# Optimization experiments

Hardware: AMD Instinct MI355X
Metric: run time of the kernel (lower is better)

The kernel has to match this reference:

```python
import jax, jax.numpy as jnp
import numpy as np

NEG_SLOPE = 0.2  # PyG GATConv default

def gat_layer(x, src, dst, W, a_src, a_dst, b, N):
    # h = W x  (PyG applies linear before attention)
    h = x @ W                                   # [N, hid]
    al_src = h @ a_src                          # [N]
    al_dst = h @ a_dst                          # [N]
    e = jax.nn.leaky_relu(al_src[src] + al_dst[dst], NEG_SLOPE)  # [E]
    # segment softmax over incoming edges of each destination node
    m = jax.ops.segment_max(e, dst, num_segments=N)
    e = jnp.exp(e - m[dst])
    s = jax.ops.segment_sum(e, dst, num_segments=N)
    coef = e / s[dst]                           # [E]
    out = jax.ops.segment_sum(h[src] * coef[:, None], dst, num_segments=N)
    return out + b

def setup_inputs() -> dict:
    key = jax.random.key(0)
    ks = jax.random.split(key, 12)
    N, E, in_dim, hid, out_dim, G = 100000, 1600000, 128, 64, 1, 256
    x = jax.random.normal(ks[0], (N, in_dim), dtype=jnp.float32)
    edge_index = jax.random.randint(ks[1], (2, E), 0, N, dtype=jnp.int64)
    batch = jnp.sort(jax.random.randint(ks[2], (N,), 0, G, dtype=jnp.int64))
    def glorot(k, shape):
        lim = float(np.sqrt(6.0 / (shape[0] + shape[-1])))
        return jax.random.uniform(k, shape, jnp.float32, -lim, lim)
    return {
        "x": x, "edge_index": edge_index, "batch": batch,
        "W1": glorot(ks[3], (in_dim, hid)),
        "a_src1": glorot(ks[4], (hid,)), "a_dst1": glorot(ks[5], (hid,)),
        "b1": jnp.zeros((hid,), jnp.float32),
        "W2": glorot(ks[6], (hid, hid)),
        "a_src2": glorot(ks[7], (hid,)), "a_dst2": glorot(ks[8], (hid,)),
        "b2": jnp.zeros((hid,), jnp.float32),
        "Wfc": glorot(ks[9], (hid, out_dim)),
        "bfc": jnp.zeros((out_dim,), jnp.float32),
    }

def reference(x, edge_index, batch, W1, a_src1, a_dst1, b1, W2, a_src2, a_dst2, b2, Wfc, bfc):
    N = x.shape[0]
    G = 256  # number of graphs in the batch
    # add self-loops (PyG GATConv default add_self_loops=True)
    loops = jnp.arange(N, dtype=edge_index.dtype)
    src = jnp.concatenate([edge_index[0], loops])
    dst = jnp.concatenate([edge_index[1], loops])
    h = jax.nn.elu(gat_layer(x, src, dst, W1, a_src1, a_dst1, b1, N))
    h = jax.nn.elu(gat_layer(h, src, dst, W2, a_src2, a_dst2, b2, N))
    # global mean pool over graph ids
    sums = jax.ops.segment_sum(h, batch, num_segments=G)
    cnts = jax.ops.segment_sum(jnp.ones((N,), h.dtype), batch, num_segments=G)
    pooled = sums / jnp.maximum(cnts, 1.0)[:, None]
    return pooled @ Wfc + bfc
```

## Files before the change

### kernel.cpp

```cpp
#include <hip/hip_runtime.h>
#include <hip/hip_bf16.h>
#include <cstdint>


#define BIN_SHIFT 8
#define BIN_NODES 256
#define PLACE_CHUNK 8192

__device__ __forceinline__ float wave_reduce_sum(float v) {
#pragma unroll
  for (int off = 32; off > 0; off >>= 1) v += __shfl_xor(v, off, 64);
  return v;
}

__device__ __forceinline__ unsigned short f2bf(float f) {
  unsigned int u = __float_as_uint(f);
  u += 0x7fffu + ((u >> 16) & 1u);
  return (unsigned short)(u >> 16);
}
__device__ __forceinline__ float bf2f(unsigned short u) {
  return __uint_as_float(((unsigned int)u) << 16);
}


__global__ void bin_count_kernel(const int* __restrict__ ei, int E, int M, int NB,
                                 int* __restrict__ binCnt) {
  extern __shared__ int hist[];
  for (int i = threadIdx.x; i < NB; i += blockDim.x) hist[i] = 0;
  __syncthreads();
  int stride = gridDim.x * blockDim.x;
  for (int t = blockIdx.x * blockDim.x + threadIdx.x; t < M; t += stride) {
    int d = (t < E) ? ei[E + t] : (t - E);
    atomicAdd(&hist[d >> BIN_SHIFT], 1);
  }
  __syncthreads();
  for (int i = threadIdx.x; i < NB; i += blockDim.x)
    if (hist[i]) atomicAdd(&binCnt[i], hist[i]);
}

__global__ void scan_bounds_kernel(const int* __restrict__ binCnt, int NB,
                                   int* __restrict__ binBase, int* __restrict__ binCursor,
                                   const int* __restrict__ batch, int* __restrict__ gstart,
                                   int N, int G) {
  if (blockIdx.x == 0) {
    int lane = threadIdx.x;
    if (lane >= 64) return;
    int per = (NB + 63) / 64;
    int vals[8];
    int base = lane * per;
    int s = 0;
#pragma unroll
    for (int i = 0; i < 8; i++) {
      int idx = base + i;
      int v = (i < per && idx < NB) ? binCnt[idx] : 0;
      vals[i] = v;
      s += v;
    }
    int x = s;
#pragma unroll
    for (int off = 1; off < 64; off <<= 1) {
      int u = __shfl_up(x, off, 64);
      if (lane >= off) x += u;
    }
    int excl = x - s;
#pragma unroll
    for (int i = 0; i < 8; i++) {
      int idx = base + i;
      if (i < per && idx < NB) {
        binBase[idx] = excl;
        binCursor[idx] = excl;
      }
      excl += vals[i];
    }
    if (lane == 63) binBase[NB] = x;
  } else {
    int g = (blockIdx.x - 1) * 256 + threadIdx.x;
    if (g > G) return;
    int lo = 0, hi = N;
    while (lo < hi) {
      int mid = (lo + hi) >> 1;
      if (batch[mid] < g) lo = mid + 1;
      else hi = mid;
    }
    gstart[g] = lo;
  }
}

__global__ __launch_bounds__(256) void bin_place_kernel(
    const int* __restrict__ ei, int E, int M, int NB,
    int* __restrict__ binCursor, int2* __restrict__ binned) {
  extern __shared__ int sh[];
  int* res = sh;
  int* cur = sh + NB;
  const int t = threadIdx.x;
  const int cbase = blockIdx.x * PLACE_CHUNK;
  const int cend = min(cbase + PLACE_CHUNK, M);

  for (int i = t; i < NB; i += 256) cur[i] = 0;
  __syncthreads();
  for (int i = cbase + t; i < cend; i += 256) {
    int d = (i < E) ? ei[E + i] : (i - E);
    atomicAdd(&cur[d >> BIN_SHIFT], 1);
  }
  __syncthreads();
  for (int i = t; i < NB; i += 256) {
    int c = cur[i];
    res[i] = c ? atomicAdd(&binCursor[i], c) : 0;
  }
  __syncthreads();
  for (int i = t; i < NB; i += 256) cur[i] = 0;
  __syncthreads();
  for (int i = cbase + t; i < cend; i += 256) {
    int s, d;
    if (i < E) { s = ei[i]; d = ei[E + i]; } else { s = d = i - E; }
    int b = d >> BIN_SHIFT;
    int r = atomicAdd(&cur[b], 1);
    binned[res[b] + r] = make_int2(s, d);
  }
}

__global__ __launch_bounds__(256) void csr_finalize_kernel(
    const int2* __restrict__ binned, const int* __restrict__ binBase,
    int* __restrict__ rowptr, int* __restrict__ csrc, int N, int NB, int M) {
  __shared__ int cnt[256];
  __shared__ int off[256];
  __shared__ int wsum[4];
  const int b = blockIdx.x;
  const int t = threadIdx.x;
  const int nodeBase = b << BIN_SHIFT;
  const int eStart = binBase[b], eEnd = binBase[b + 1];

  cnt[t] = 0;
  __syncthreads();
  for (int i = eStart + t; i < eEnd; i += 256) {
    atomicAdd(&cnt[binned[i].y - nodeBase], 1);
  }
  __syncthreads();
  {
    int lane = t & 63, wv = t >> 6;
    int v = cnt[t];
    int x = v;
#pragma unroll
    for (int o = 1; o < 64; o <<= 1) {
      int u = __shfl_up(x, o, 64);
      if (lane >= o) x += u;
    }
    if (lane == 63) wsum[wv] = x;
    __syncthreads();
    int woff = 0;
    for (int j = 0; j < wv; j++) woff += wsum[j];
    off[t] = woff + x - v;
  }
  __syncthreads();
  int node = nodeBase + t;
  if (node < N) rowptr[node] = eStart + off[t];
  if (b == NB - 1 && t == 0) rowptr[N] = M;
  cnt[t] = off[t];
  __syncthreads();
  for (int i = eStart + t; i < eEnd; i += 256) {
    int2 e = binned[i];
    int r = atomicAdd(&cnt[e.y - nodeBase], 1);
    csrc[eStart + r] = e.x;
  }
}


template <int KDIM>
__global__ __launch_bounds__(256) void gemm64(const float* __restrict__ A,
                                              const float* __restrict__ W,
                                              unsigned short* __restrict__ hb,
                                              const float* __restrict__ a_src,
                                              const float* __restrict__ a_dst,
                                              float* __restrict__ alsrc,
                                              float* __restrict__ aldst, int N) {
  __shared__ float As[32][68];
  __shared__ float Ws[32][68];
  const int block_m = blockIdx.x * 64;
  const int t = threadIdx.x;
  const int tc = t & 15;
  const int tr = t >> 4;
  const int c0 = tc * 4, r0 = tr * 4;
  float acc[4][4] = {};

  for (int kc = 0; kc < KDIM; kc += 32) {
    for (int q = t; q < 512; q += 256) {
      int node = q >> 3, f4 = q & 7;
      int gn = block_m + node;
      if (gn >= N) gn = N - 1;
      const float4 v = *(const float4*)(A + (size_t)gn * KDIM + kc + f4 * 4);
      As[f4 * 4 + 0][node] = v.x;
      As[f4 * 4 + 1][node] = v.y;
      As[f4 * 4 + 2][node] = v.z;
      As[f4 * 4 + 3][node] = v.w;
    }
    for (int q = t; q < 512; q += 256) {
      int k = q >> 4, f4 = q & 15;
      const float4 v = *(const float4*)(W + (size_t)(kc + k) * 64 + f4 * 4);
      *(float4*)&Ws[k][f4 * 4] = v;
    }
    __syncthreads();
#pragma unroll
    for (int k = 0; k < 32; ++k) {
      float4 a = *(const float4*)&As[k][r0];
      float4 b = *(const float4*)&Ws[k][c0];
      acc[0][0] += a.x * b.x; acc[0][1] += a.x * b.y; acc[0][2] += a.x * b.z; acc[0][3] += a.x * b.w;
      acc[1][0] += a.y * b.x; acc[1][1] += a.y * b.y; acc[1][2] += a.y * b.z; acc[1][3] += a.y * b.w;
      acc[2][0] += a.z * b.x; acc[2][1] += a.z * b.y; acc[2][2] += a.z * b.z; acc[2][3] += a.z * b.w;
      acc[3][0] += a.w * b.x; acc[3][1] += a.w * b.y; acc[3][2] += a.w * b.z; acc[3][3] += a.w * b.w;
    }
    __syncthreads();
  }

  const float as0 = a_src[c0], as1 = a_src[c0 + 1], as2 = a_src[c0 + 2], as3 = a_src[c0 + 3];
  const float ad0 = a_dst[c0], ad1 = a_dst[c0 + 1], ad2 = a_dst[c0 + 2], ad3 = a_dst[c0 + 3];
#pragma unroll
  for (int i = 0; i < 4; ++i) {
    int gn = block_m + r0 + i;
    if (gn < N) {
      ushort4 u;
      u.x = f2bf(acc[i][0]); u.y = f2bf(acc[i][1]);
      u.z = f2bf(acc[i][2]); u.w = f2bf(acc[i][3]);
      *(ushort4*)(hb + (size_t)gn * 64 + c0) = u;
    }
    float ps = acc[i][0] * as0 + acc[i][1] * as1 + acc[i][2] * as2 + acc[i][3] * as3;
    float pd = acc[i][0] * ad0 + acc[i][1] * ad1 + acc[i][2] * ad2 + acc[i][3] * ad3;
#pragma unroll
    for (int off = 1; off < 16; off <<= 1) {
      ps += __shfl_xor(ps, off, 64);
      pd += __shfl_xor(pd, off, 64);
    }
    if (tc == 0 && gn < N) {
      alsrc[gn] = ps;
      aldst[gn] = pd;
    }
  }
}

template <int ELU>
__global__ __launch_bounds__(256) void spmm_fused_kernel(
    const int* __restrict__ rowptr, const int* __restrict__ csrc,
    const float* __restrict__ alsrc, const float* __restrict__ aldst,
    const unsigned short* __restrict__ hb, const float* __restrict__ bias,
    float* __restrict__ outbuf, int N) {
  const int t = threadIdx.x;
  const int l = t & 15;
  const int gb = t & 48;
  const int node = blockIdx.x * 16 + (t >> 4);
  if (node >= N) return;
  const int start = rowptr[node];
  const int end = rowptr[node + 1];
  const float ad = aldst[node];

  float m = -1e30f;
  float ssum = 0.f;
  float4 acc0 = make_float4(0.f, 0.f, 0.f, 0.f);
  float4 acc1 = make_float4(0.f, 0.f, 0.f, 0.f);
  float4 acc2 = make_float4(0.f, 0.f, 0.f, 0.f);
  float4 acc3 = make_float4(0.f, 0.f, 0.f, 0.f);

  for (int base = start; base < end; base += 16) {
    int i = base + l;
    bool valid = i < end;
    int s = valid ? csrc[i] : 0;
    float al = alsrc[s];

    ushort4 u[16];
#pragma unroll
    for (int j = 0; j < 16; ++j) {
      int sj = __shfl(s, gb + j, 64);
      u[j] = *(const ushort4*)(hb + (size_t)sj * 64 + l * 4);
    }

    float e = al + ad;
    e = (e > 0.f) ? e : 0.2f * e;
    if (!valid) e = -1e30f;
    float cmax = e;
#pragma unroll
    for (int off = 1; off < 16; off <<= 1) cmax = fmaxf(cmax, __shfl_xor(cmax, off, 64));
    float newm = fmaxf(m, cmax);
    float scale = __expf(m - newm);
    float w = valid ? __expf(e - newm) : 0.f;
    float wsum = w;
#pragma unroll
    for (int off = 1; off < 16; off <<= 1) wsum += __shfl_xor(wsum, off, 64);
    ssum = ssum * scale + wsum;
    acc0.x *= scale; acc0.y *= scale; acc0.z *= scale; acc0.w *= scale;
    acc1.x *= scale; acc1.y *= scale; acc1.z *= scale; acc1.w *= scale;
    acc2.x *= scale; acc2.y *= scale; acc2.z *= scale; acc2.w *= scale;
    acc3.x *= scale; acc3.y *= scale; acc3.z *= scale; acc3.w *= scale;
    m = newm;

#pragma unroll
    for (int j = 0; j < 16; ++j) {
      float wj = __shfl(w, gb + j, 64);
      float4* A = ((j & 3) == 0) ? &acc0 : ((j & 3) == 1) ? &acc1
                : ((j & 3) == 2) ? &acc2 : &acc3;
      A->x += wj * bf2f(u[j].x);
      A->y += wj * bf2f(u[j].y);
      A->z += wj * bf2f(u[j].z);
      A->w += wj * bf2f(u[j].w);
    }
  }

  float inv = 1.0f / ssum;
  float4 r;
  r.x = ((acc0.x + acc1.x) + (acc2.x + acc3.x)) * inv;
  r.y = ((acc0.y + acc1.y) + (acc2.y + acc3.y)) * inv;
  r.z = ((acc0.z + acc1.z) + (acc2.z + acc3.z)) * inv;
  r.w = ((acc0.w + acc1.w) + (acc2.w + acc3.w)) * inv;
  if (ELU) {
    const float4 b4 = *(const float4*)(bias + l * 4);
    r.x += b4.x; r.y += b4.y; r.z += b4.z; r.w += b4.w;
    r.x = (r.x > 0.f) ? r.x : expm1f(r.x);
    r.y = (r.y > 0.f) ? r.y : expm1f(r.y);
    r.z = (r.z > 0.f) ? r.z : expm1f(r.z);
    r.w = (r.w > 0.f) ? r.w : expm1f(r.w);
  }
  *(float4*)(outbuf + (size_t)node * 64 + l * 4) = r;
}

__global__ __launch_bounds__(256) void post_pool_kernel(
    const float* __restrict__ acc, const float* __restrict__ bias,
    const int* __restrict__ batch, float* __restrict__ pool, int N) {
  __shared__ float4 red4[16][17];
  __shared__ int sB[16];
  __shared__ int uni;
  const int t = threadIdx.x;
  const int ln = t >> 4;
  const int f4 = t & 15;
  const int base = blockIdx.x * 16;
  const int node = base + ln;

  if (t < 16) {
    int nn = base + t;
    sB[t] = (nn < N) ? batch[nn] : -1;
  }
  __syncthreads();
  if (t == 0) {
    int u = (base + 15 < N);
    for (int i = 1; i < 16; i++) u &= (sB[i] == sB[0]);
    uni = u;
  }

  float4 v = make_float4(0.f, 0.f, 0.f, 0.f);
  if (node < N) {
    v = *(const float4*)(acc + ((size_t)node * 16 + f4) * 4);
    const float4 b4 = *(const float4*)(bias + f4 * 4);
    v.x += b4.x; v.y += b4.y; v.z += b4.z; v.w += b4.w;
    v.x = (v.x > 0.f) ? v.x : expm1f(v.x);
    v.y = (v.y > 0.f) ? v.y : expm1f(v.y);
    v.z = (v.z > 0.f) ? v.z : expm1f(v.z);
    v.w = (v.w > 0.f) ? v.w : expm1f(v.w);
  }
  red4[ln][f4] = v;
  __syncthreads();

  if (t < 64) {
    const float* rf = (const float*)red4;
    if (uni) {
      float s = 0.f;
#pragma unroll
      for (int n = 0; n < 16; n++) s += rf[n * 68 + t];
      atomicAdd(&pool[(size_t)sB[0] * 64 + t], s);
    } else {
      for (int n = 0; n < 16; n++) {
        int g = sB[n];
        if (g >= 0) atomicAdd(&pool[(size_t)g * 64 + t], rf[n * 68 + t]);
      }
    }
  }
}

__global__ void final_kernel(const float* __restrict__ pool, const int* __restrict__ gstart,
                             const float* __restrict__ Wfc, const float* __restrict__ bfc,
                             float* __restrict__ out, int G) {
  int wid = (blockIdx.x * blockDim.x + threadIdx.x) >> 6;
  int lane = threadIdx.x & 63;
  if (wid >= G) return;
  float c = (float)max(gstart[wid + 1] - gstart[wid], 1);
  float v = pool[(size_t)wid * 64 + lane] * (1.0f / c) * Wfc[lane];
  v = wave_reduce_sum(v);
  if (lane == 0) out[wid] = v + bfc[0];
}


extern "C" void kernel_launch(void* const* d_in, const int* in_sizes, int n_in,
                              void* d_out, int out_size, void* d_ws, size_t ws_size,
                              hipStream_t stream) {
  const float* x     = (const float*)d_in[0];
  const int*   ei    = (const int*)d_in[1];
  const int*   batch = (const int*)d_in[2];
  const float* W1    = (const float*)d_in[3];
  const float* asrc1 = (const float*)d_in[4];
  const float* adst1 = (const float*)d_in[5];
  const float* b1    = (const float*)d_in[6];
  const float* W2    = (const float*)d_in[7];
  const float* asrc2 = (const float*)d_in[8];
  const float* adst2 = (const float*)d_in[9];
  const float* b2    = (const float*)d_in[10];
  const float* Wfc   = (const float*)d_in[11];
  const float* bfc   = (const float*)d_in[12];
  float* out = (float*)d_out;

  const int N = in_sizes[0] / 128;
  const int E = in_sizes[1] / 2;
  const int G = 256;
  const int M = E + N;
  const int NB = (N + BIN_NODES - 1) >> BIN_SHIFT;

  char* p = (char*)d_ws;
  auto alloc = [&](size_t bytes) {
    char* r = p;
    p += (bytes + 255) & ~size_t(255);
    return r;
  };
  float*          h1e    = (float*)alloc((size_t)N * 64 * 4);
  float*          accbuf = (float*)alloc((size_t)N * 64 * 4);
  unsigned short* hb     = (unsigned short*)alloc((size_t)N * 64 * 2);
  float* alsrc  = (float*)alloc((size_t)N * 4);
  float* aldst  = (float*)alloc((size_t)N * 4);
  int*   rowptr = (int*)alloc((size_t)(N + 1) * 4);
  int*   csrc   = (int*)alloc((size_t)M * 4);
  int2*  binned = (int2*)alloc((size_t)M * 8);
  int*   binCnt = (int*)alloc((size_t)NB * 4);
  int*   binBase = (int*)alloc((size_t)(NB + 1) * 4);
  int*   binCursor = (int*)alloc((size_t)NB * 4);
  float* pool   = (float*)alloc((size_t)G * 64 * 4);
  int*   gstart = (int*)alloc((size_t)(G + 1) * 4);

  hipMemsetAsync(binCnt, 0, (size_t)NB * 4, stream);
  bin_count_kernel<<<512, 256, NB * 4, stream>>>(ei, E, M, NB, binCnt);
  scan_bounds_kernel<<<3, 256, 0, stream>>>(binCnt, NB, binBase, binCursor,
                                            batch, gstart, N, G);
  bin_place_kernel<<<(M + PLACE_CHUNK - 1) / PLACE_CHUNK, 256, 2 * NB * 4, stream>>>(
      ei, E, M, NB, binCursor, binned);
  csr_finalize_kernel<<<NB, 256, 0, stream>>>(binned, binBase, rowptr, csrc, N, NB, M);

  gemm64<128><<<(N + 63) / 64, 256, 0, stream>>>(x, W1, hb, asrc1, adst1, alsrc, aldst, N);
  spmm_fused_kernel<1><<<(N + 15) / 16, 256, 0, stream>>>(rowptr, csrc, alsrc, aldst,
                                                          hb, b1, h1e, N);

  gemm64<64><<<(N + 63) / 64, 256, 0, stream>>>(h1e, W2, hb, asrc2, adst2, alsrc, aldst, N);
  spmm_fused_kernel<0><<<(N + 15) / 16, 256, 0, stream>>>(rowptr, csrc, alsrc, aldst,
                                                          hb, nullptr, accbuf, N);
  hipMemsetAsync(pool, 0, (size_t)G * 64 * 4, stream);
  post_pool_kernel<<<(N + 15) / 16, 256, 0, stream>>>(accbuf, b2, batch, pool, N);

  final_kernel<<<(G * 64 + 255) / 256, 256, 0, stream>>>(pool, gstart, Wfc, bfc, out, G);
}
```

Before: 311.6 us.

## Fuse layer-2 pooling into SpMM, pack binned edges, split full/tail chunks

New measurement: 334.7 us. 7.4% more time.

```diff
diff --git a/kernel.cpp b/kernel.cpp
--- a/kernel.cpp
+++ b/kernel.cpp
@@ -88,7 +88,7 @@
 
 __global__ __launch_bounds__(256) void bin_place_kernel(
     const int* __restrict__ ei, int E, int M, int NB,
-    int* __restrict__ binCursor, int2* __restrict__ binned) {
+    int* __restrict__ binCursor, unsigned int* __restrict__ binned) {
   extern __shared__ int sh[];
   int* res = sh;
   int* cur = sh + NB;
@@ -115,12 +115,12 @@
     if (i < E) { s = ei[i]; d = ei[E + i]; } else { s = d = i - E; }
     int b = d >> BIN_SHIFT;
     int r = atomicAdd(&cur[b], 1);
-    binned[res[b] + r] = make_int2(s, d);
+    binned[res[b] + r] = ((unsigned int)(d & (BIN_NODES - 1)) << 24) | (unsigned int)s;
   }
 }
 
 __global__ __launch_bounds__(256) void csr_finalize_kernel(
-    const int2* __restrict__ binned, const int* __restrict__ binBase,
+    const unsigned int* __restrict__ binned, const int* __restrict__ binBase,
     int* __restrict__ rowptr, int* __restrict__ csrc, int N, int NB, int M) {
   __shared__ int cnt[256];
   __shared__ int off[256];
@@ -133,7 +133,7 @@
   cnt[t] = 0;
   __syncthreads();
   for (int i = eStart + t; i < eEnd; i += 256) {
-    atomicAdd(&cnt[binned[i].y - nodeBase], 1);
+    atomicAdd(&cnt[binned[i] >> 24], 1);
   }
   __syncthreads();
   {
@@ -158,9 +158,9 @@
   cnt[t] = off[t];
   __syncthreads();
   for (int i = eStart + t; i < eEnd; i += 256) {
-    int2 e = binned[i];
-    int r = atomicAdd(&cnt[e.y - nodeBase], 1);
-    csrc[eStart + r] = e.x;
+    unsigned int pk = binned[i];
+    int r = atomicAdd(&cnt[pk >> 24], 1);
+    csrc[eStart + r] = (int)(pk & 0xFFFFFFu);
   }
 }
 
@@ -236,79 +236,127 @@
   }
 }
 
-template <int ELU>
+template <int POOL>
 __global__ __launch_bounds__(256) void spmm_fused_kernel(
     const int* __restrict__ rowptr, const int* __restrict__ csrc,
     const float* __restrict__ alsrc, const float* __restrict__ aldst,
     const unsigned short* __restrict__ hb, const float* __restrict__ bias,
-    float* __restrict__ outbuf, int N) {
+    float* __restrict__ outbuf, const int* __restrict__ batch,
+    float* __restrict__ pool, int N) {
   const int t = threadIdx.x;
   const int l = t & 15;
   const int gb = t & 48;
   const int node = blockIdx.x * 16 + (t >> 4);
-  if (node >= N) return;
-  const int start = rowptr[node];
-  const int end = rowptr[node + 1];
-  const float ad = aldst[node];
-
-  float m = -1e30f;
-  float ssum = 0.f;
-  float4 acc0 = make_float4(0.f, 0.f, 0.f, 0.f);
-  float4 acc1 = make_float4(0.f, 0.f, 0.f, 0.f);
-  float4 acc2 = make_float4(0.f, 0.f, 0.f, 0.f);
-  float4 acc3 = make_float4(0.f, 0.f, 0.f, 0.f);
-
-  for (int base = start; base < end; base += 16) {
-    int i = base + l;
-    bool valid = i < end;
-    int s = valid ? csrc[i] : 0;
-    float al = alsrc[s];
-
-    ushort4 u[16];
-#pragma unroll
-    for (int j = 0; j < 16; ++j) {
-      int sj = __shfl(s, gb + j, 64);
-      u[j] = *(const ushort4*)(hb + (size_t)sj * 64 + l * 4);
-    }
-
-    float e = al + ad;
-    e = (e > 0.f) ? e : 0.2f * e;
-    if (!valid) e = -1e30f;
-    float cmax = e;
-#pragma unroll
-    for (int off = 1; off < 16; off <<= 1) cmax = fmaxf(cmax, __shfl_xor(cmax, off, 64));
-    float newm = fmaxf(m, cmax);
-    float scale = __expf(m - newm);
-    float w = valid ? __expf(e - newm) : 0.f;
-    float wsum = w;
-#pragma unroll
-    for (int off = 1; off < 16; off <<= 1) wsum += __shfl_xor(wsum, off, 64);
-    ssum = ssum * scale + wsum;
-    acc0.x *= scale; acc0.y *= scale; acc0.z *= scale; acc0.w *= scale;
-    acc1.x *= scale; acc1.y *= scale; acc1.z *= scale; acc1.w *= scale;
-    acc2.x *= scale; acc2.y *= scale; acc2.z *= scale; acc2.w *= scale;
-    acc3.x *= scale; acc3.y *= scale; acc3.z *= scale; acc3.w *= scale;
-    m = newm;
-
-#pragma unroll
-    for (int j = 0; j < 16; ++j) {
-      float wj = __shfl(w, gb + j, 64);
-      float4* A = ((j & 3) == 0) ? &acc0 : ((j & 3) == 1) ? &acc1
-                : ((j & 3) == 2) ? &acc2 : &acc3;
-      A->x += wj * bf2f(u[j].x);
-      A->y += wj * bf2f(u[j].y);
-      A->z += wj * bf2f(u[j].z);
-      A->w += wj * bf2f(u[j].w);
-    }
-  }
-
-  float inv = 1.0f / ssum;
-  float4 r;
-  r.x = ((acc0.x + acc1.x) + (acc2.x + acc3.x)) * inv;
-  r.y = ((acc0.y + acc1.y) + (acc2.y + acc3.y)) * inv;
-  r.z = ((acc0.z + acc1.z) + (acc2.z + acc3.z)) * inv;
-  r.w = ((acc0.w + acc1.w) + (acc2.w + acc3.w)) * inv;
-  if (ELU) {
+  const bool active = node < N;
+
+  float4 r = make_float4(0.f, 0.f, 0.f, 0.f);
+  if (active) {
+    const int start = rowptr[node];
+    const int end = rowptr[node + 1];
+    const float ad = aldst[node];
+
+    float m = -1e30f;
+    float ssum = 0.f;
+    float4 acc0 = make_float4(0.f, 0.f, 0.f, 0.f);
+    float4 acc1 = make_float4(0.f, 0.f, 0.f, 0.f);
+    float4 acc2 = make_float4(0.f, 0.f, 0.f, 0.f);
+    float4 acc3 = make_float4(0.f, 0.f, 0.f, 0.f);
+
+    int base = start;
+    for (; base + 16 <= end; base += 16) {
+      int s = csrc[base + l];
+      float al = alsrc[s];
+
+      ushort4 u[16];
+#pragma unroll
+      for (int j = 0; j < 16; ++j) {
+        int sj = __shfl(s, gb + j, 64);
+        u[j] = *(const ushort4*)(hb + (size_t)sj * 64 + l * 4);
+      }
+
+      float e = al + ad;
+      e = (e > 0.f) ? e : 0.2f * e;
+      float cmax = e;
+#pragma unroll
+      for (int off = 1; off < 16; off <<= 1) cmax = fmaxf(cmax, __shfl_xor(cmax, off, 64));
+      float newm = fmaxf(m, cmax);
+      float scale = __expf(m - newm);
+      float w = __expf(e - newm);
+      float wsum = w;
+#pragma unroll
+      for (int off = 1; off < 16; off <<= 1) wsum += __shfl_xor(wsum, off, 64);
+      ssum = ssum * scale + wsum;
+      acc0.x *= scale; acc0.y *= scale; acc0.z *= scale; acc0.w *= scale;
+      acc1.x *= scale; acc1.y *= scale; acc1.z *= scale; acc1.w *= scale;
+      acc2.x *= scale; acc2.y *= scale; acc2.z *= scale; acc2.w *= scale;
+      acc3.x *= scale; acc3.y *= scale; acc3.z *= scale; acc3.w *= scale;
+      m = newm;
+
+#pragma unroll
+      for (int j = 0; j < 16; ++j) {
+        float wj = __shfl(w, gb + j, 64);
+        float4* A = ((j & 3) == 0) ? &acc0 : ((j & 3) == 1) ? &acc1
+                  : ((j & 3) == 2) ? &acc2 : &acc3;
+        A->x += wj * bf2f(u[j].x);
+        A->y += wj * bf2f(u[j].y);
+        A->z += wj * bf2f(u[j].z);
+        A->w += wj * bf2f(u[j].w);
+      }
+    }
+
+    if (base < end) {
+      int i = base + l;
+      bool valid = i < end;
+      int s = valid ? csrc[i] : 0;
+      float al = alsrc[s];
+
+      float e = al + ad;
+      e = (e > 0.f) ? e : 0.2f * e;
+      if (!valid) e = -1e30f;
+      float cmax = e;
+#pragma unroll
+      for (int off = 1; off < 16; off <<= 1) cmax = fmaxf(cmax, __shfl_xor(cmax, off, 64));
+      float newm = fmaxf(m, cmax);
+      float scale = __expf(m - newm);
+      float w = valid ? __expf(e - newm) : 0.f;
+      float wsum = w;
+#pragma unroll
+      for (int off = 1; off < 16; off <<= 1) wsum += __shfl_xor(wsum, off, 64);
+      ssum = ssum * scale + wsum;
+      acc0.x *= scale; acc0.y *= scale; acc0.z *= scale; acc0.w *= scale;
+      acc1.x *= scale; acc1.y *= scale; acc1.z *= scale; acc1.w *= scale;
+      acc2.x *= scale; acc2.y *= scale; acc2.z *= scale; acc2.w *= scale;
+      acc3.x *= scale; acc3.y *= scale; acc3.z *= scale; acc3.w *= scale;
+      m = newm;
+
+#pragma unroll
+      for (int jb = 0; jb < 16; jb += 4) {
+        if (base + jb < end) {
+          ushort4 u[4];
+          float wj[4];
+#pragma unroll
+          for (int j = 0; j < 4; ++j) {
+            int sj = __shfl(s, gb + jb + j, 64);
+            wj[j] = __shfl(w, gb + jb + j, 64);
+            u[j] = *(const ushort4*)(hb + (size_t)sj * 64 + l * 4);
+          }
+#pragma unroll
+          for (int j = 0; j < 4; ++j) {
+            float4* A = (j == 0) ? &acc0 : (j == 1) ? &acc1 : (j == 2) ? &acc2 : &acc3;
+            A->x += wj[j] * bf2f(u[j].x);
+            A->y += wj[j] * bf2f(u[j].y);
+            A->z += wj[j] * bf2f(u[j].z);
+            A->w += wj[j] * bf2f(u[j].w);
+          }
+        }
+      }
+    }
+
+    float inv = 1.0f / ssum;
+    r.x = ((acc0.x + acc1.x) + (acc2.x + acc3.x)) * inv;
+    r.y = ((acc0.y + acc1.y) + (acc2.y + acc3.y)) * inv;
+    r.z = ((acc0.z + acc1.z) + (acc2.z + acc3.z)) * inv;
+    r.w = ((acc0.w + acc1.w) + (acc2.w + acc3.w)) * inv;
     const float4 b4 = *(const float4*)(bias + l * 4);
     r.x += b4.x; r.y += b4.y; r.z += b4.z; r.w += b4.w;
     r.x = (r.x > 0.f) ? r.x : expm1f(r.x);
@@ -316,56 +364,39 @@
     r.z = (r.z > 0.f) ? r.z : expm1f(r.z);
     r.w = (r.w > 0.f) ? r.w : expm1f(r.w);
   }
-  *(float4*)(outbuf + (size_t)node * 64 + l * 4) = r;
-}
-
-__global__ __launch_bounds__(256) void post_pool_kernel(
-    const float* __restrict__ acc, const float* __restrict__ bias,
-    const int* __restrict__ batch, float* __restrict__ pool, int N) {
-  __shared__ float4 red4[16][17];
-  __shared__ int sB[16];
-  __shared__ int uni;
-  const int t = threadIdx.x;
-  const int ln = t >> 4;
-  const int f4 = t & 15;
-  const int base = blockIdx.x * 16;
-  const int node = base + ln;
-
-  if (t < 16) {
-    int nn = base + t;
-    sB[t] = (nn < N) ? batch[nn] : -1;
-  }
-  __syncthreads();
-  if (t == 0) {
-    int u = (base + 15 < N);
-    for (int i = 1; i < 16; i++) u &= (sB[i] == sB[0]);
-    uni = u;
-  }
-
-  float4 v = make_float4(0.f, 0.f, 0.f, 0.f);
-  if (node < N) {
-    v = *(const float4*)(acc + ((size_t)node * 16 + f4) * 4);
-    const float4 b4 = *(const float4*)(bias + f4 * 4);
-    v.x += b4.x; v.y += b4.y; v.z += b4.z; v.w += b4.w;
-    v.x = (v.x > 0.f) ? v.x : expm1f(v.x);
-    v.y = (v.y > 0.f) ? v.y : expm1f(v.y);
-    v.z = (v.z > 0.f) ? v.z : expm1f(v.z);
-    v.w = (v.w > 0.f) ? v.w : expm1f(v.w);
-  }
-  red4[ln][f4] = v;
-  __syncthreads();
-
-  if (t < 64) {
-    const float* rf = (const float*)red4;
-    if (uni) {
-      float s = 0.f;
-#pragma unroll
-      for (int n = 0; n < 16; n++) s += rf[n * 68 + t];
-      atomicAdd(&pool[(size_t)sB[0] * 64 + t], s);
-    } else {
-      for (int n = 0; n < 16; n++) {
-        int g = sB[n];
-        if (g >= 0) atomicAdd(&pool[(size_t)g * 64 + t], rf[n * 68 + t]);
+
+  if (!POOL) {
+    if (active) *(float4*)(outbuf + (size_t)node * 64 + l * 4) = r;
+  } else {
+    __shared__ float4 red4[16][17];
+    __shared__ int sB[16];
+    __shared__ int uni;
+    const int blkBase = blockIdx.x * 16;
+    if (t < 16) {
+      int nn = blkBase + t;
+      sB[t] = (nn < N) ? batch[nn] : -1;
+    }
+    __syncthreads();
+    if (t == 0) {
+      int u = (blkBase + 15 < N);
+      for (int i = 1; i < 16; i++) u &= (sB[i] == sB[0]);
+      uni = u;
+    }
+    if (!active) r = make_float4(0.f, 0.f, 0.f, 0.f);
+    red4[t >> 4][l] = r;
+    __syncthreads();
+    if (t < 64) {
+      const float* rf = (const float*)red4;
+      if (uni) {
+        float sum = 0.f;
+#pragma unroll
+        for (int n = 0; n < 16; n++) sum += rf[n * 68 + t];
+        atomicAdd(&pool[(size_t)sB[0] * 64 + t], sum);
+      } else {
+        for (int n = 0; n < 16; n++) {
+          int g = sB[n];
+          if (g >= 0) atomicAdd(&pool[(size_t)g * 64 + t], rf[n * 68 + t]);
+        }
       }
     }
   }
@@ -415,13 +446,12 @@
     return r;
   };
   float*          h1e    = (float*)alloc((size_t)N * 64 * 4);
-  float*          accbuf = (float*)alloc((size_t)N * 64 * 4);
   unsigned short* hb     = (unsigned short*)alloc((size_t)N * 64 * 2);
   float* alsrc  = (float*)alloc((size_t)N * 4);
   float* aldst  = (float*)alloc((size_t)N * 4);
   int*   rowptr = (int*)alloc((size_t)(N + 1) * 4);
   int*   csrc   = (int*)alloc((size_t)M * 4);
-  int2*  binned = (int2*)alloc((size_t)M * 8);
+  unsigned int* binned = (unsigned int*)alloc((size_t)M * 4);
   int*   binCnt = (int*)alloc((size_t)NB * 4);
   int*   binBase = (int*)alloc((size_t)(NB + 1) * 4);
   int*   binCursor = (int*)alloc((size_t)NB * 4);
@@ -437,14 +467,13 @@
   csr_finalize_kernel<<<NB, 256, 0, stream>>>(binned, binBase, rowptr, csrc, N, NB, M);
 
   gemm64<128><<<(N + 63) / 64, 256, 0, stream>>>(x, W1, hb, asrc1, adst1, alsrc, aldst, N);
+  spmm_fused_kernel<0><<<(N + 15) / 16, 256, 0, stream>>>(rowptr, csrc, alsrc, aldst,
+                                                          hb, b1, h1e, nullptr, nullptr, N);
+
+  gemm64<64><<<(N + 63) / 64, 256, 0, stream>>>(h1e, W2, hb, asrc2, adst2, alsrc, aldst, N);
+  hipMemsetAsync(pool, 0, (size_t)G * 64 * 4, stream);
   spmm_fused_kernel<1><<<(N + 15) / 16, 256, 0, stream>>>(rowptr, csrc, alsrc, aldst,
-                                                          hb, b1, h1e, N);
-
-  gemm64<64><<<(N + 63) / 64, 256, 0, stream>>>(h1e, W2, hb, asrc2, adst2, alsrc, aldst, N);
-  spmm_fused_kernel<0><<<(N + 15) / 16, 256, 0, stream>>>(rowptr, csrc, alsrc, aldst,
-                                                          hb, nullptr, accbuf, N);
-  hipMemsetAsync(pool, 0, (size_t)G * 64 * 4, stream);
-  post_pool_kernel<<<(N + 15) / 16, 256, 0, stream>>>(accbuf, b2, batch, pool, N);
+                                                          hb, b2, nullptr, batch, pool, N);
 
   final_kernel<<<(G * 64 + 255) / 256, 256, 0, stream>>>(pool, gstart, Wfc, bfc, out, G);
 }
```

## Replace counted CSR build with fixed-capacity bins and packed edge records

Applied to the files above, without the earlier changes.

Result: faster. 293.3 us (-5.9%).

```diff
diff --git a/kernel.cpp b/kernel.cpp
--- a/kernel.cpp
+++ b/kernel.cpp
@@ -5,7 +5,8 @@
 
 #define BIN_SHIFT 8
 #define BIN_NODES 256
-#define PLACE_CHUNK 8192
+#define BIN_CAP 6144
+#define PLACE_CHUNK 2048
 
 __device__ __forceinline__ float wave_reduce_sum(float v) {
 #pragma unroll
@@ -23,84 +24,32 @@
 }
 
 
-__global__ void bin_count_kernel(const int* __restrict__ ei, int E, int M, int NB,
-                                 int* __restrict__ binCnt) {
-  extern __shared__ int hist[];
-  for (int i = threadIdx.x; i < NB; i += blockDim.x) hist[i] = 0;
-  __syncthreads();
-  int stride = gridDim.x * blockDim.x;
-  for (int t = blockIdx.x * blockDim.x + threadIdx.x; t < M; t += stride) {
-    int d = (t < E) ? ei[E + t] : (t - E);
-    atomicAdd(&hist[d >> BIN_SHIFT], 1);
-  }
-  __syncthreads();
-  for (int i = threadIdx.x; i < NB; i += blockDim.x)
-    if (hist[i]) atomicAdd(&binCnt[i], hist[i]);
-}
-
-__global__ void scan_bounds_kernel(const int* __restrict__ binCnt, int NB,
-                                   int* __restrict__ binBase, int* __restrict__ binCursor,
-                                   const int* __restrict__ batch, int* __restrict__ gstart,
-                                   int N, int G) {
-  if (blockIdx.x == 0) {
-    int lane = threadIdx.x;
-    if (lane >= 64) return;
-    int per = (NB + 63) / 64;
-    int vals[8];
-    int base = lane * per;
-    int s = 0;
-#pragma unroll
-    for (int i = 0; i < 8; i++) {
-      int idx = base + i;
-      int v = (i < per && idx < NB) ? binCnt[idx] : 0;
-      vals[i] = v;
-      s += v;
-    }
-    int x = s;
-#pragma unroll
-    for (int off = 1; off < 64; off <<= 1) {
-      int u = __shfl_up(x, off, 64);
-      if (lane >= off) x += u;
-    }
-    int excl = x - s;
-#pragma unroll
-    for (int i = 0; i < 8; i++) {
-      int idx = base + i;
-      if (i < per && idx < NB) {
-        binBase[idx] = excl;
-        binCursor[idx] = excl;
-      }
-      excl += vals[i];
-    }
-    if (lane == 63) binBase[NB] = x;
-  } else {
-    int g = (blockIdx.x - 1) * 256 + threadIdx.x;
-    if (g > G) return;
-    int lo = 0, hi = N;
-    while (lo < hi) {
-      int mid = (lo + hi) >> 1;
-      if (batch[mid] < g) lo = mid + 1;
-      else hi = mid;
-    }
-    gstart[g] = lo;
-  }
-}
-
 __global__ __launch_bounds__(256) void bin_place_kernel(
     const int* __restrict__ ei, int E, int M, int NB,
-    int* __restrict__ binCursor, int2* __restrict__ binned) {
-  extern __shared__ int sh[];
-  int* res = sh;
-  int* cur = sh + NB;
+    int* __restrict__ binCursor, unsigned int* __restrict__ binned) {
+  __shared__ int cur[512];
+  __shared__ int res[512];
   const int t = threadIdx.x;
   const int cbase = blockIdx.x * PLACE_CHUNK;
-  const int cend = min(cbase + PLACE_CHUNK, M);
 
   for (int i = t; i < NB; i += 256) cur[i] = 0;
   __syncthreads();
-  for (int i = cbase + t; i < cend; i += 256) {
-    int d = (i < E) ? ei[E + i] : (i - E);
-    atomicAdd(&cur[d >> BIN_SHIFT], 1);
+
+  unsigned int pk[PLACE_CHUNK / 256];
+  int br[PLACE_CHUNK / 256];
+#pragma unroll
+  for (int j = 0; j < PLACE_CHUNK / 256; ++j) {
+    int i = cbase + t + j * 256;
+    if (i < M) {
+      int s, d;
+      if (i < E) { s = ei[i]; d = ei[E + i]; } else { s = d = i - E; }
+      int b = d >> BIN_SHIFT;
+      int r = atomicAdd(&cur[b], 1);
+      pk[j] = ((unsigned int)(d & (BIN_NODES - 1)) << 24) | (unsigned int)s;
+      br[j] = (b << 16) | r;
+    } else {
+      br[j] = -1;
+    }
   }
   __syncthreads();
   for (int i = t; i < NB; i += 256) {
@@ -108,37 +57,38 @@
     res[i] = c ? atomicAdd(&binCursor[i], c) : 0;
   }
   __syncthreads();
-  for (int i = t; i < NB; i += 256) cur[i] = 0;
-  __syncthreads();
-  for (int i = cbase + t; i < cend; i += 256) {
-    int s, d;
-    if (i < E) { s = ei[i]; d = ei[E + i]; } else { s = d = i - E; }
-    int b = d >> BIN_SHIFT;
-    int r = atomicAdd(&cur[b], 1);
-    binned[res[b] + r] = make_int2(s, d);
+#pragma unroll
+  for (int j = 0; j < PLACE_CHUNK / 256; ++j) {
+    if (br[j] >= 0) {
+      int b = br[j] >> 16;
+      int pos = res[b] + (br[j] & 0xFFFF);
+      if (pos < BIN_CAP) binned[(size_t)b * BIN_CAP + pos] = pk[j];
+    }
   }
 }
 
 __global__ __launch_bounds__(256) void csr_finalize_kernel(
-    const int2* __restrict__ binned, const int* __restrict__ binBase,
-    int* __restrict__ rowptr, int* __restrict__ csrc, int N, int NB, int M) {
+    const unsigned int* __restrict__ binned, const int* __restrict__ binCursor,
+    int* __restrict__ rowbeg, int* __restrict__ rowend, int* __restrict__ csrc,
+    int N, int NB) {
   __shared__ int cnt[256];
   __shared__ int off[256];
   __shared__ int wsum[4];
   const int b = blockIdx.x;
   const int t = threadIdx.x;
   const int nodeBase = b << BIN_SHIFT;
-  const int eStart = binBase[b], eEnd = binBase[b + 1];
+  const int eBase = b * BIN_CAP;
+  const int cntE = binCursor[b];
 
   cnt[t] = 0;
   __syncthreads();
-  for (int i = eStart + t; i < eEnd; i += 256) {
-    atomicAdd(&cnt[binned[i].y - nodeBase], 1);
-  }
-  __syncthreads();
+  for (int i = t; i < cntE; i += 256) {
+    atomicAdd(&cnt[binned[eBase + i] >> 24], 1);
+  }
+  __syncthreads();
+  int v = cnt[t];
   {
     int lane = t & 63, wv = t >> 6;
-    int v = cnt[t];
     int x = v;
 #pragma unroll
     for (int o = 1; o < 64; o <<= 1) {
@@ -153,15 +103,30 @@
   }
   __syncthreads();
   int node = nodeBase + t;
-  if (node < N) rowptr[node] = eStart + off[t];
-  if (b == NB - 1 && t == 0) rowptr[N] = M;
+  if (node < N) {
+    rowbeg[node] = eBase + off[t];
+    rowend[node] = eBase + off[t] + v;
+  }
   cnt[t] = off[t];
   __syncthreads();
-  for (int i = eStart + t; i < eEnd; i += 256) {
-    int2 e = binned[i];
-    int r = atomicAdd(&cnt[e.y - nodeBase], 1);
-    csrc[eStart + r] = e.x;
-  }
+  for (int i = t; i < cntE; i += 256) {
+    unsigned int pk = binned[eBase + i];
+    int r = atomicAdd(&cnt[pk >> 24], 1);
+    csrc[eBase + r] = (int)(pk & 0xFFFFFFu);
+  }
+}
+
+__global__ void bounds_kernel(const int* __restrict__ batch, int* __restrict__ gstart,
+                              int N, int G) {
+  int g = blockIdx.x * blockDim.x + threadIdx.x;
+  if (g > G) return;
+  int lo = 0, hi = N;
+  while (lo < hi) {
+    int mid = (lo + hi) >> 1;
+    if (batch[mid] < g) lo = mid + 1;
+    else hi = mid;
+  }
+  gstart[g] = lo;
 }
 
 
@@ -238,7 +203,8 @@
 
 template <int ELU>
 __global__ __launch_bounds__(256) void spmm_fused_kernel(
-    const int* __restrict__ rowptr, const int* __restrict__ csrc,
+    const int* __restrict__ rowbeg, const int* __restrict__ rowend,
+    const int* __restrict__ csrc,
     const float* __restrict__ alsrc, const float* __restrict__ aldst,
     const unsigned short* __restrict__ hb, const float* __restrict__ bias,
     float* __restrict__ outbuf, int N) {
@@ -247,8 +213,8 @@
   const int gb = t & 48;
   const int node = blockIdx.x * 16 + (t >> 4);
   if (node >= N) return;
-  const int start = rowptr[node];
-  const int end = rowptr[node + 1];
+  const int start = rowbeg[node];
+  const int end = rowend[node];
   const float ad = aldst[node];
 
   float m = -1e30f;
@@ -419,30 +385,28 @@
   unsigned short* hb     = (unsigned short*)alloc((size_t)N * 64 * 2);
   float* alsrc  = (float*)alloc((size_t)N * 4);
   float* aldst  = (float*)alloc((size_t)N * 4);
-  int*   rowptr = (int*)alloc((size_t)(N + 1) * 4);
-  int*   csrc   = (int*)alloc((size_t)M * 4);
-  int2*  binned = (int2*)alloc((size_t)M * 8);
-  int*   binCnt = (int*)alloc((size_t)NB * 4);
-  int*   binBase = (int*)alloc((size_t)(NB + 1) * 4);
+  int*   rowbeg = (int*)alloc((size_t)N * 4);
+  int*   rowend = (int*)alloc((size_t)N * 4);
+  int*   csrc   = (int*)alloc((size_t)NB * BIN_CAP * 4);
+  unsigned int* binned = (unsigned int*)alloc((size_t)NB * BIN_CAP * 4);
   int*   binCursor = (int*)alloc((size_t)NB * 4);
   float* pool   = (float*)alloc((size_t)G * 64 * 4);
   int*   gstart = (int*)alloc((size_t)(G + 1) * 4);
 
-  hipMemsetAsync(binCnt, 0, (size_t)NB * 4, stream);
-  bin_count_kernel<<<512, 256, NB * 4, stream>>>(ei, E, M, NB, binCnt);
-  scan_bounds_kernel<<<3, 256, 0, stream>>>(binCnt, NB, binBase, binCursor,
-                                            batch, gstart, N, G);
-  bin_place_kernel<<<(M + PLACE_CHUNK - 1) / PLACE_CHUNK, 256, 2 * NB * 4, stream>>>(
+  hipMemsetAsync(binCursor, 0, (size_t)NB * 4, stream);
+  bin_place_kernel<<<(M + PLACE_CHUNK - 1) / PLACE_CHUNK, 256, 0, stream>>>(
       ei, E, M, NB, binCursor, binned);
-  csr_finalize_kernel<<<NB, 256, 0, stream>>>(binned, binBase, rowptr, csrc, N, NB, M);
+  csr_finalize_kernel<<<NB, 256, 0, stream>>>(binned, binCursor, rowbeg, rowend,
+                                              csrc, N, NB);
+  bounds_kernel<<<2, 256, 0, stream>>>(batch, gstart, N, G);
 
   gemm64<128><<<(N + 63) / 64, 256, 0, stream>>>(x, W1, hb, asrc1, adst1, alsrc, aldst, N);
-  spmm_fused_kernel<1><<<(N + 15) / 16, 256, 0, stream>>>(rowptr, csrc, alsrc, aldst,
-                                                          hb, b1, h1e, N);
+  spmm_fused_kernel<1><<<(N + 15) / 16, 256, 0, stream>>>(rowbeg, rowend, csrc, alsrc,
+                                                          aldst, hb, b1, h1e, N);
 
   gemm64<64><<<(N + 63) / 64, 256, 0, stream>>>(h1e, W2, hb, asrc2, adst2, alsrc, aldst, N);
-  spmm_fused_kernel<0><<<(N + 15) / 16, 256, 0, stream>>>(rowptr, csrc, alsrc, aldst,
-                                                          hb, nullptr, accbuf, N);
+  spmm_fused_kernel<0><<<(N + 15) / 16, 256, 0, stream>>>(rowbeg, rowend, csrc, alsrc,
+                                                          aldst, hb, nullptr, accbuf, N);
   hipMemsetAsync(pool, 0, (size_t)G * 64 * 4, stream);
   post_pool_kernel<<<(N + 15) / 16, 256, 0, stream>>>(accbuf, b2, batch, pool, N);
 
```
